# Kernel tuning notes

Measured on AMD Instinct MI355X. Metric: run time of the kernel, lower is better.

## Reference

```python
import jax, jax.numpy as jnp
import numpy as np


def setup_inputs() -> dict:
    key = jax.random.key(0)
    ks = jax.random.split(key, 6)
    N, E, D = 50000, 500000, 128
    H, O = 256, 128
    x = jax.random.normal(ks[0], (N, D), dtype=jnp.float32)
    edge_attr = jax.random.normal(ks[1], (E, D), dtype=jnp.float32)
    edge_index = jax.random.randint(ks[2], (E, 2), 0, N, dtype=jnp.int64)
    # MLP params, scaled like torch default init
    W1 = jax.random.normal(ks[3], (3 * D, H), dtype=jnp.float32) / np.sqrt(3 * D)
    b1 = jnp.zeros((H,), dtype=jnp.float32)
    W2 = jax.random.normal(ks[4], (H, O), dtype=jnp.float32) / np.sqrt(H)
    b2 = jnp.zeros((O,), dtype=jnp.float32)
    return {"x": x, "edge_attr": edge_attr, "W1": W1, "b1": b1,
            "W2": W2, "b2": b2, "edge_index": edge_index}


def reference(x, edge_attr, W1, b1, W2, b2, edge_index):
    # edge_index: [E, 2]; column 0 = sender, column 1 = receiver
    sender = x[edge_index[:, 0]]    # [E, D] gather
    receiver = x[edge_index[:, 1]]  # [E, D] gather
    feat = jnp.concatenate([sender, receiver, edge_attr], axis=-1)  # [E, 3D]
    h = jax.nn.relu(feat @ W1 + b1)  # [E, H]
    return h @ W2 + b2               # [E, O]
```

## Files before the change

kernel.cpp:

```cpp
#include <hip/hip_runtime.h>
#include <hip/hip_bf16.h>

#define D 128
#define K1 384
#define H 256
#define O 128
#define BE 64
#define GRIDP 256
#define LDF (K1 + 8)
#define LDHF (H + 8)

typedef __attribute__((ext_vector_type(8))) short bf16x8;
typedef __attribute__((ext_vector_type(4))) float f32x4;

#define SSW(row, col) ((row) * 128 + ((col) ^ (((row) & 7) << 3)))
#define HSW(row, col) ((row) * 256 + ((col) ^ (((row) & 7) << 3)))

#define LGKM_BARRIER()                                                 \
    do {                                                               \
        asm volatile("s_waitcnt lgkmcnt(0)\n\ts_barrier" ::: "memory");\
        __builtin_amdgcn_sched_barrier(0);                             \
    } while (0)

__device__ inline ushort f2b(float f) {
    union { float f; unsigned u; } v; v.f = f;
    unsigned u = v.u;
    unsigned r = (u + 0x7fffu + ((u >> 16) & 1u)) >> 16;
    return (ushort)r;
}
__device__ inline ushort4 cvt4(float4 v) {
    ushort4 u; u.x = f2b(v.x); u.y = f2b(v.y); u.z = f2b(v.z); u.w = f2b(v.w); return u;
}
__device__ inline bf16x8 cvt8(f32x4 a, f32x4 b) {
    union { bf16x8 v; ushort u[8]; } w;
    w.u[0] = f2b(a[0]); w.u[1] = f2b(a[1]); w.u[2] = f2b(a[2]); w.u[3] = f2b(a[3]);
    w.u[4] = f2b(b[0]); w.u[5] = f2b(b[1]); w.u[6] = f2b(b[2]); w.u[7] = f2b(b[3]);
    return w.v;
}

__global__ void prep_weights(const float* __restrict__ W1, const float* __restrict__ W2,
                             ushort* __restrict__ W1t, ushort* __restrict__ W2t) {
    int tid = blockIdx.x * blockDim.x + threadIdx.x;
    if (tid < 256 * 384) {
        int n = tid / 384, k = tid % 384;
        W1t[tid] = f2b(W1[k * 256 + n]);
    } else {
        int t2 = tid - 256 * 384;
        if (t2 < 128 * 256) {
            int o = t2 / 256, k = t2 % 256;
            W2t[t2] = f2b(W2[k * 128 + o]);
        }
    }
}

__global__ __launch_bounds__(256)
void prep_x(const float* __restrict__ x, ushort* __restrict__ Xb, long total8) {
    long t = (long)blockIdx.x * blockDim.x + threadIdx.x;
    if (t < total8) {
        const float* src = x + t * 8;
        float4 v0 = ((const float4*)src)[0], v1 = ((const float4*)src)[1];
        union { bf16x8 v; ushort4 u[2]; } w;
        w.u[0] = cvt4(v0); w.u[1] = cvt4(v1);
        *(bf16x8*)(Xb + t * 8) = w.v;
    }
}

__global__ __launch_bounds__(512, 2)
void edge_mlp13(const float* __restrict__ ea, const int* __restrict__ eidx,
                const ushort* __restrict__ Xb,
                const ushort* __restrict__ W1t, const ushort* __restrict__ W2t,
                const float* __restrict__ b1, const float* __restrict__ b2,
                float* __restrict__ out, int E, int ntiles) {
    __shared__ __align__(16) ushort sBuf[24576];
    ushort* s0 = sBuf;
    ushort* s1 = sBuf + 8192;
    ushort* s2 = sBuf + 16384;
    ushort* sH = sBuf;

    const int tid = threadIdx.x;
    const int wave = tid >> 6, lane = tid & 63;
    const int row16 = lane & 15, kgrp = lane >> 4;
    const int srow = tid >> 3, oct = tid & 7;

    bf16x8 w1f[12][2];
    #pragma unroll
    for (int ks = 0; ks < 12; ++ks)
        #pragma unroll
        for (int fc = 0; fc < 2; ++fc)
            w1f[ks][fc] = *(const bf16x8*)(W1t + (wave * 32 + fc * 16 + row16) * K1 + ks * 32 + kgrp * 8);
    bf16x8 w2f[8];
    #pragma unroll
    for (int ks = 0; ks < 8; ++ks)
        w2f[ks] = *(const bf16x8*)(W2t + (wave * 16 + row16) * H + ks * 32 + kgrp * 8);
    float4 b1q[2];
    #pragma unroll
    for (int fc = 0; fc < 2; ++fc)
        b1q[fc] = *(const float4*)(b1 + wave * 32 + fc * 16 + kgrp * 4);
    const float b2v = b2[wave * 16 + row16];

    int t = blockIdx.x;
    if (t >= ntiles) return;

    bf16x8 pxs[2], pxr[2];
    f32x4  pea[4];

    {
        long se = (long)t * BE + srow; if (se >= E) se = E - 1;
        int2 ei = *(const int2*)(eidx + 2 * se);
        const ushort* ps = Xb + (long)ei.x * D + oct * 16;
        const ushort* pr = Xb + (long)ei.y * D + oct * 16;
        const float*  pe = ea + se * D + oct * 16;
        #pragma unroll
        for (int j = 0; j < 2; ++j) pxs[j] = *(const bf16x8*)(ps + j * 8);
        #pragma unroll
        for (int j = 0; j < 2; ++j) pxr[j] = *(const bf16x8*)(pr + j * 8);
        #pragma unroll
        for (int j = 0; j < 4; ++j) pea[j] = ((const f32x4*)pe)[j];

        #pragma unroll
        for (int j = 0; j < 2; ++j) *(bf16x8*)(s0 + SSW(srow, oct * 16 + j * 8)) = pxs[j];
        #pragma unroll
        for (int j = 0; j < 2; ++j) *(bf16x8*)(s1 + SSW(srow, oct * 16 + j * 8)) = pxr[j];
        *(bf16x8*)(s2 + SSW(srow, oct * 16 + 0)) = cvt8(pea[0], pea[1]);
        *(bf16x8*)(s2 + SSW(srow, oct * 16 + 8)) = cvt8(pea[2], pea[3]);
    }

    int tn = t + GRIDP;
    int2 ei2;
    {
        int tc = (tn < ntiles) ? tn : (ntiles - 1);
        long se = (long)tc * BE + srow; if (se >= E) se = E - 1;
        ei2 = *(const int2*)(eidx + 2 * se);
    }

    while (true) {
        LGKM_BARRIER();
        const bool hasNext = (tn < ntiles);
        if (hasNext) {
            long sen = (long)tn * BE + srow; if (sen >= E) sen = E - 1;
            const ushort* ps = Xb + (long)ei2.x * D + oct * 16;
            const ushort* pr = Xb + (long)ei2.y * D + oct * 16;
            const float*  pe = ea + sen * D + oct * 16;
            #pragma unroll
            for (int j = 0; j < 2; ++j) pxs[j] = *(const bf16x8*)(ps + j * 8);
            #pragma unroll
            for (int j = 0; j < 2; ++j) pxr[j] = *(const bf16x8*)(pr + j * 8);
            #pragma unroll
            for (int j = 0; j < 4; ++j) pea[j] = ((const f32x4*)pe)[j];
            int tnn = tn + GRIDP;
            int tc = (tnn < ntiles) ? tnn : (ntiles - 1);
            long se2 = (long)tc * BE + srow; if (se2 >= E) se2 = E - 1;
            ei2 = *(const int2*)(eidx + 2 * se2);
        }

        f32x4 acc[4][2];
        #pragma unroll
        for (int fe = 0; fe < 4; ++fe) { acc[fe][0] = (f32x4){0,0,0,0}; acc[fe][1] = (f32x4){0,0,0,0}; }

        #pragma unroll
        for (int ks = 0; ks < 12; ++ks) {
            const ushort* sA = (ks < 4) ? s0 : ((ks < 8) ? s1 : s2);
            const int kl = (ks & 3) * 32 + kgrp * 8;
            bf16x8 a[4];
            #pragma unroll
            for (int fe = 0; fe < 4; ++fe)
                a[fe] = *(const bf16x8*)(sA + SSW(fe * 16 + row16, kl));
            #pragma unroll
            for (int fe = 0; fe < 4; ++fe) {
                acc[fe][0] = __builtin_amdgcn_mfma_f32_16x16x32_bf16(w1f[ks][0], a[fe], acc[fe][0], 0, 0, 0);
                acc[fe][1] = __builtin_amdgcn_mfma_f32_16x16x32_bf16(w1f[ks][1], a[fe], acc[fe][1], 0, 0, 0);
            }
        }
        LGKM_BARRIER();

        #pragma unroll
        for (int fe = 0; fe < 4; ++fe) {
            int erow = fe * 16 + row16;
            int base = erow * 256;
            int swz = (erow & 7) << 3;
            #pragma unroll
            for (int fc = 0; fc < 2; ++fc) {
                int colb = wave * 32 + fc * 16 + kgrp * 4;
                ushort4 u;
                u.x = f2b(fmaxf(acc[fe][fc][0] + b1q[fc].x, 0.f));
                u.y = f2b(fmaxf(acc[fe][fc][1] + b1q[fc].y, 0.f));
                u.z = f2b(fmaxf(acc[fe][fc][2] + b1q[fc].z, 0.f));
                u.w = f2b(fmaxf(acc[fe][fc][3] + b1q[fc].w, 0.f));
                *(ushort4*)(sH + base + (colb ^ swz)) = u;
            }
        }
        LGKM_BARRIER();

        f32x4 acc2[4];
        #pragma unroll
        for (int fr = 0; fr < 4; ++fr) acc2[fr] = (f32x4){0,0,0,0};
        #pragma unroll
        for (int ks = 0; ks < 8; ++ks) {
            bf16x8 a[4];
            #pragma unroll
            for (int fr = 0; fr < 4; ++fr)
                a[fr] = *(const bf16x8*)(sH + HSW(fr * 16 + row16, ks * 32 + kgrp * 8));
            #pragma unroll
            for (int fr = 0; fr < 4; ++fr)
                acc2[fr] = __builtin_amdgcn_mfma_f32_16x16x32_bf16(a[fr], w2f[ks], acc2[fr], 0, 0, 0);
        }
        {
            const long e0 = (long)t * BE;
            #pragma unroll
            for (int fr = 0; fr < 4; ++fr)
                #pragma unroll
                for (int r = 0; r < 4; ++r) {
                    long erow = e0 + fr * 16 + kgrp * 4 + r;
                    if (erow < E) out[erow * O + wave * 16 + row16] = acc2[fr][r] + b2v;
                }
        }

        if (!hasNext) break;
        LGKM_BARRIER();
        #pragma unroll
        for (int j = 0; j < 2; ++j) *(bf16x8*)(s0 + SSW(srow, oct * 16 + j * 8)) = pxs[j];
        #pragma unroll
        for (int j = 0; j < 2; ++j) *(bf16x8*)(s1 + SSW(srow, oct * 16 + j * 8)) = pxr[j];
        *(bf16x8*)(s2 + SSW(srow, oct * 16 + 0)) = cvt8(pea[0], pea[1]);
        *(bf16x8*)(s2 + SSW(srow, oct * 16 + 8)) = cvt8(pea[2], pea[3]);

        t = tn; tn += GRIDP;
    }
}

__global__ __launch_bounds__(256, 2)
void edge_mlp(const float* __restrict__ x, const float* __restrict__ ea,
              const int* __restrict__ eidx,
              const float* __restrict__ b1, const float* __restrict__ b2,
              const ushort* __restrict__ W1t, const ushort* __restrict__ W2t,
              float* __restrict__ out, int E) {
    __shared__ ushort sF[64 * LDF];
    ushort* sH = sF;
    const int tid = threadIdx.x, wave = tid >> 6, lane = tid & 63;
    const int row16 = lane & 15, kgrp = lane >> 4;
    const long e0 = (long)blockIdx.x * 64;
    {
        int i = tid >> 2, p = tid & 3;
        long e = e0 + i; if (e >= E) e = E - 1;
        int s = eidx[2 * e], r = eidx[2 * e + 1];
        const float* src0 = x + (long)s * D + p * 32;
        const float* src1 = x + (long)r * D + p * 32;
        const float* src2 = ea + e * D + p * 32;
        ushort* dst = sF + i * LDF + p * 32;
        #pragma unroll
        for (int j = 0; j < 8; ++j) *(ushort4*)(dst + 0 * D + j * 4) = cvt4(((const float4*)src0)[j]);
        #pragma unroll
        for (int j = 0; j < 8; ++j) *(ushort4*)(dst + 1 * D + j * 4) = cvt4(((const float4*)src1)[j]);
        #pragma unroll
        for (int j = 0; j < 8; ++j) *(ushort4*)(dst + 2 * D + j * 4) = cvt4(((const float4*)src2)[j]);
    }
    __syncthreads();
    f32x4 acc[4][4];
    #pragma unroll
    for (int a = 0; a < 4; ++a)
        #pragma unroll
        for (int b = 0; b < 4; ++b) acc[a][b] = (f32x4){0,0,0,0};
    const int wcol = wave * 64;
    for (int k0 = 0; k0 < K1; k0 += 32) {
        bf16x8 a[4], b[4];
        #pragma unroll
        for (int fr = 0; fr < 4; ++fr)
            a[fr] = *(const bf16x8*)(sF + (fr * 16 + row16) * LDF + k0 + kgrp * 8);
        #pragma unroll
        for (int fc = 0; fc < 4; ++fc)
            b[fc] = *(const bf16x8*)(W1t + (wcol + fc * 16 + row16) * K1 + k0 + kgrp * 8);
        #pragma unroll
        for (int fr = 0; fr < 4; ++fr)
            #pragma unroll
            for (int fc = 0; fc < 4; ++fc)
                acc[fr][fc] = __builtin_amdgcn_mfma_f32_16x16x32_bf16(a[fr], b[fc], acc[fr][fc], 0, 0, 0);
    }
    __syncthreads();
    #pragma unroll
    for (int fc = 0; fc < 4; ++fc) {
        int col = wcol + fc * 16 + row16;
        float bv = b1[col];
        #pragma unroll
        for (int fr = 0; fr < 4; ++fr)
            #pragma unroll
            for (int r = 0; r < 4; ++r) {
                int row = fr * 16 + kgrp * 4 + r;
                sH[row * LDHF + col] = f2b(fmaxf(acc[fr][fc][r] + bv, 0.f));
            }
    }
    __syncthreads();
    f32x4 acc2[4][2];
    #pragma unroll
    for (int a = 0; a < 4; ++a)
        #pragma unroll
        for (int b = 0; b < 2; ++b) acc2[a][b] = (f32x4){0,0,0,0};
    const int wo = wave * 32;
    for (int k0 = 0; k0 < H; k0 += 32) {
        bf16x8 a[4], b[2];
        #pragma unroll
        for (int fr = 0; fr < 4; ++fr)
            a[fr] = *(const bf16x8*)(sH + (fr * 16 + row16) * LDHF + k0 + kgrp * 8);
        #pragma unroll
        for (int fc = 0; fc < 2; ++fc)
            b[fc] = *(const bf16x8*)(W2t + (wo + fc * 16 + row16) * H + k0 + kgrp * 8);
        #pragma unroll
        for (int fr = 0; fr < 4; ++fr)
            #pragma unroll
            for (int fc = 0; fc < 2; ++fc)
                acc2[fr][fc] = __builtin_amdgcn_mfma_f32_16x16x32_bf16(a[fr], b[fc], acc2[fr][fc], 0, 0, 0);
    }
    #pragma unroll
    for (int fc = 0; fc < 2; ++fc) {
        int col = wo + fc * 16 + row16;
        float bv = b2[col];
        #pragma unroll
        for (int fr = 0; fr < 4; ++fr)
            #pragma unroll
            for (int r = 0; r < 4; ++r) {
                long row = e0 + fr * 16 + kgrp * 4 + r;
                if (row < E) out[row * O + col] = acc2[fr][fc][r] + bv;
            }
    }
}

extern "C" void kernel_launch(void* const* d_in, const int* in_sizes, int n_in,
                              void* d_out, int out_size, void* d_ws, size_t ws_size,
                              hipStream_t stream) {
    const float* x  = (const float*)d_in[0];
    const float* ea = (const float*)d_in[1];
    const float* W1 = (const float*)d_in[2];
    const float* b1 = (const float*)d_in[3];
    const float* W2 = (const float*)d_in[4];
    const float* b2 = (const float*)d_in[5];
    const int* eidx = (const int*)d_in[6];
    float* out = (float*)d_out;

    const int E = in_sizes[1] / D;
    const int N = in_sizes[0] / D;

    ushort* W1t = (ushort*)d_ws;
    ushort* W2t = W1t + 256 * 384;
    ushort* Xb  = W2t + 128 * 256;
    size_t need = ((size_t)(256 * 384 + 128 * 256) + (size_t)N * 128) * 2;

    prep_weights<<<512, 256, 0, stream>>>(W1, W2, W1t, W2t);

    if (ws_size >= need) {
        long total8 = (long)N * D / 8;
        int nbx = (int)((total8 + 255) / 256);
        prep_x<<<nbx, 256, 0, stream>>>(x, Xb, total8);
        int ntiles = (E + BE - 1) / BE;
        int grid = (ntiles < GRIDP) ? ntiles : GRIDP;
        edge_mlp13<<<grid, 512, 0, stream>>>(ea, eidx, Xb, W1t, W2t, b1, b2, out, E, ntiles);
    } else {
        int nb = (E + 63) / 64;
        edge_mlp<<<nb, 256, 0, stream>>>(x, ea, eidx, b1, b2, W1t, W2t, out, E);
    }
}
```

Baseline: 210.6 us.

## Software-pipeline GEMM2 of previous tile with GEMM1 using double-buffered LDS

Restructures the persistent edge-MLP loop so the second GEMM and output store for the previous tile run in the same phase as the first GEMM of the current tile. Input feature staging is double-buffered in LDS and the hidden buffer gets its own region, which removes two barriers per tile. LDS use per block grows from 48KB to 128KB, which may stop two 512-thread blocks from sharing a CU and so lower occupancy despite the launch bounds.

Result: slower. 233.6 us (+10.9%).

```diff
diff --git a/kernel.cpp b/kernel.cpp
--- a/kernel.cpp
+++ b/kernel.cpp
@@ -66,16 +66,13 @@
 }
 
 __global__ __launch_bounds__(512, 2)
-void edge_mlp13(const float* __restrict__ ea, const int* __restrict__ eidx,
+void edge_mlp14(const float* __restrict__ ea, const int* __restrict__ eidx,
                 const ushort* __restrict__ Xb,
                 const ushort* __restrict__ W1t, const ushort* __restrict__ W2t,
                 const float* __restrict__ b1, const float* __restrict__ b2,
                 float* __restrict__ out, int E, int ntiles) {
-    __shared__ __align__(16) ushort sBuf[24576];
-    ushort* s0 = sBuf;
-    ushort* s1 = sBuf + 8192;
-    ushort* s2 = sBuf + 16384;
-    ushort* sH = sBuf;
+    __shared__ __align__(16) ushort sBuf[65536];
+    ushort* sH = sBuf + 49152;
 
     const int tid = threadIdx.x;
     const int wave = tid >> 6, lane = tid & 63;
@@ -118,13 +115,15 @@
         for (int j = 0; j < 4; ++j) pea[j] = ((const f32x4*)pe)[j];
 
         #pragma unroll
-        for (int j = 0; j < 2; ++j) *(bf16x8*)(s0 + SSW(srow, oct * 16 + j * 8)) = pxs[j];
-        #pragma unroll
-        for (int j = 0; j < 2; ++j) *(bf16x8*)(s1 + SSW(srow, oct * 16 + j * 8)) = pxr[j];
-        *(bf16x8*)(s2 + SSW(srow, oct * 16 + 0)) = cvt8(pea[0], pea[1]);
-        *(bf16x8*)(s2 + SSW(srow, oct * 16 + 8)) = cvt8(pea[2], pea[3]);
-    }
-
+        for (int j = 0; j < 2; ++j) *(bf16x8*)(sBuf + SSW(srow, oct * 16 + j * 8)) = pxs[j];
+        #pragma unroll
+        for (int j = 0; j < 2; ++j) *(bf16x8*)(sBuf + 8192 + SSW(srow, oct * 16 + j * 8)) = pxr[j];
+        *(bf16x8*)(sBuf + 16384 + SSW(srow, oct * 16 + 0)) = cvt8(pea[0], pea[1]);
+        *(bf16x8*)(sBuf + 16384 + SSW(srow, oct * 16 + 8)) = cvt8(pea[2], pea[3]);
+    }
+
+    int p = 0;
+    int tprev = -1;
     int tn = t + GRIDP;
     int2 ei2;
     {
@@ -133,7 +132,7 @@
         ei2 = *(const int2*)(eidx + 2 * se);
     }
 
-    while (true) {
+    for (;;) {
         LGKM_BARRIER();
         const bool hasNext = (tn < ntiles);
         if (hasNext) {
@@ -153,24 +152,62 @@
             ei2 = *(const int2*)(eidx + 2 * se2);
         }
 
+        f32x4 acc2[4];
+        if (tprev >= 0) {
+            #pragma unroll
+            for (int fr = 0; fr < 4; ++fr) acc2[fr] = (f32x4){0,0,0,0};
+            #pragma unroll
+            for (int ks = 0; ks < 8; ++ks) {
+                bf16x8 a[4];
+                #pragma unroll
+                for (int fr = 0; fr < 4; ++fr)
+                    a[fr] = *(const bf16x8*)(sH + HSW(fr * 16 + row16, ks * 32 + kgrp * 8));
+                #pragma unroll
+                for (int fr = 0; fr < 4; ++fr)
+                    acc2[fr] = __builtin_amdgcn_mfma_f32_16x16x32_bf16(a[fr], w2f[ks], acc2[fr], 0, 0, 0);
+            }
+        }
+
+        const ushort* sA = sBuf + (p ? 24576 : 0);
         f32x4 acc[4][2];
         #pragma unroll
         for (int fe = 0; fe < 4; ++fe) { acc[fe][0] = (f32x4){0,0,0,0}; acc[fe][1] = (f32x4){0,0,0,0}; }
-
         #pragma unroll
         for (int ks = 0; ks < 12; ++ks) {
-            const ushort* sA = (ks < 4) ? s0 : ((ks < 8) ? s1 : s2);
+            const ushort* sP = sA + ((ks < 4) ? 0 : ((ks < 8) ? 8192 : 16384));
             const int kl = (ks & 3) * 32 + kgrp * 8;
             bf16x8 a[4];
             #pragma unroll
             for (int fe = 0; fe < 4; ++fe)
-                a[fe] = *(const bf16x8*)(sA + SSW(fe * 16 + row16, kl));
+                a[fe] = *(const bf16x8*)(sP + SSW(fe * 16 + row16, kl));
             #pragma unroll
             for (int fe = 0; fe < 4; ++fe) {
                 acc[fe][0] = __builtin_amdgcn_mfma_f32_16x16x32_bf16(w1f[ks][0], a[fe], acc[fe][0], 0, 0, 0);
                 acc[fe][1] = __builtin_amdgcn_mfma_f32_16x16x32_bf16(w1f[ks][1], a[fe], acc[fe][1], 0, 0, 0);
             }
         }
+
+        if (tprev >= 0) {
+            const long e0p = (long)tprev * BE;
+            #pragma unroll
+            for (int fr = 0; fr < 4; ++fr)
+                #pragma unroll
+                for (int r = 0; r < 4; ++r) {
+                    long erow = e0p + fr * 16 + kgrp * 4 + r;
+                    if (erow < E) out[erow * O + wave * 16 + row16] = acc2[fr][r] + b2v;
+                }
+        }
+
+        if (hasNext) {
+            ushort* sB = sBuf + (p ? 0 : 24576);
+            #pragma unroll
+            for (int j = 0; j < 2; ++j) *(bf16x8*)(sB + SSW(srow, oct * 16 + j * 8)) = pxs[j];
+            #pragma unroll
+            for (int j = 0; j < 2; ++j) *(bf16x8*)(sB + 8192 + SSW(srow, oct * 16 + j * 8)) = pxr[j];
+            *(bf16x8*)(sB + 16384 + SSW(srow, oct * 16 + 0)) = cvt8(pea[0], pea[1]);
+            *(bf16x8*)(sB + 16384 + SSW(srow, oct * 16 + 8)) = cvt8(pea[2], pea[3]);
+        }
+
         LGKM_BARRIER();
 
         #pragma unroll
@@ -189,8 +226,14 @@
                 *(ushort4*)(sH + base + (colb ^ swz)) = u;
             }
         }
-        LGKM_BARRIER();
-
+
+        tprev = t; t = tn; tn += GRIDP;
+        if (t >= ntiles) break;
+        p ^= 1;
+    }
+
+    LGKM_BARRIER();
+    {
         f32x4 acc2[4];
         #pragma unroll
         for (int fr = 0; fr < 4; ++fr) acc2[fr] = (f32x4){0,0,0,0};
@@ -204,27 +247,14 @@
             for (int fr = 0; fr < 4; ++fr)
                 acc2[fr] = __builtin_amdgcn_mfma_f32_16x16x32_bf16(a[fr], w2f[ks], acc2[fr], 0, 0, 0);
         }
-        {
-            const long e0 = (long)t * BE;
-            #pragma unroll
-            for (int fr = 0; fr < 4; ++fr)
-                #pragma unroll
-                for (int r = 0; r < 4; ++r) {
-                    long erow = e0 + fr * 16 + kgrp * 4 + r;
-                    if (erow < E) out[erow * O + wave * 16 + row16] = acc2[fr][r] + b2v;
-                }
-        }
-
-        if (!hasNext) break;
-        LGKM_BARRIER();
-        #pragma unroll
-        for (int j = 0; j < 2; ++j) *(bf16x8*)(s0 + SSW(srow, oct * 16 + j * 8)) = pxs[j];
-        #pragma unroll
-        for (int j = 0; j < 2; ++j) *(bf16x8*)(s1 + SSW(srow, oct * 16 + j * 8)) = pxr[j];
-        *(bf16x8*)(s2 + SSW(srow, oct * 16 + 0)) = cvt8(pea[0], pea[1]);
-        *(bf16x8*)(s2 + SSW(srow, oct * 16 + 8)) = cvt8(pea[2], pea[3]);
-
-        t = tn; tn += GRIDP;
+        const long e0p = (long)tprev * BE;
+        #pragma unroll
+        for (int fr = 0; fr < 4; ++fr)
+            #pragma unroll
+            for (int r = 0; r < 4; ++r) {
+                long erow = e0p + fr * 16 + kgrp * 4 + r;
+                if (erow < E) out[erow * O + wave * 16 + row16] = acc2[fr][r] + b2v;
+            }
     }
 }
 
@@ -351,7 +381,7 @@
         prep_x<<<nbx, 256, 0, stream>>>(x, Xb, total8);
         int ntiles = (E + BE - 1) / BE;
         int grid = (ntiles < GRIDP) ? ntiles : GRIDP;
-        edge_mlp13<<<grid, 512, 0, stream>>>(ea, eidx, Xb, W1t, W2t, b1, b2, out, E, ntiles);
+        edge_mlp14<<<grid, 512, 0, stream>>>(ea, eidx, Xb, W1t, W2t, b1, b2, out, E, ntiles);
     } else {
         int nb = (E + 63) / 64;
         edge_mlp<<<nb, 256, 0, stream>>>(x, ea, eidx, b1, b2, W1t, W2t, out, E);
```
